# Kernel tuning notes

Measured on AMD Instinct MI355X. Metric: run time of the kernel, lower is better.

The kernel has to match this reference:

```python
import jax, jax.numpy as jnp
import numpy as np

HIDDEN = 2560
N_HEADS = 8
N_KV = 4
HEAD_DIM = 256
SLIDING_WINDOW = 512
SOFTCAP = 50.0
EPS = 1e-6
ROPE_BASE = 10000.0


def setup_inputs() -> dict:
    key = jax.random.key(0)
    ks = jax.random.split(key, 6)
    B, L = 2, 2048
    x = jax.random.normal(ks[0], (B, L, HIDDEN), dtype=jnp.float32)
    mask = jnp.zeros((1, 1, L, L), dtype=jnp.float32)  # additive attention mask
    s = 0.02
    q_w = jax.random.normal(ks[1], (N_HEADS * HEAD_DIM, HIDDEN), dtype=jnp.float32) * s
    k_w = jax.random.normal(ks[2], (N_KV * HEAD_DIM, HIDDEN), dtype=jnp.float32) * s
    v_w = jax.random.normal(ks[3], (N_KV * HEAD_DIM, HIDDEN), dtype=jnp.float32) * s
    o_w = jax.random.normal(ks[4], (HIDDEN, N_HEADS * HEAD_DIM), dtype=jnp.float32) * s
    # Gemma RMSNorm scale initialized to zero (acts as (1 + w))
    q_norm_w = jnp.zeros((HEAD_DIM,), dtype=jnp.float32)
    k_norm_w = jnp.zeros((HEAD_DIM,), dtype=jnp.float32)
    return {"x": x, "mask": mask, "q_w": q_w, "k_w": k_w, "v_w": v_w,
            "o_w": o_w, "q_norm_w": q_norm_w, "k_norm_w": k_norm_w}


def rms_norm(x, w):
    x32 = x.astype(jnp.float32)
    normed = x32 * jax.lax.rsqrt(jnp.mean(x32 * x32, axis=-1, keepdims=True) + EPS)
    return (normed * (1.0 + w)).astype(x.dtype)


def rope_cos_sin(L):
    inv_freq = 1.0 / (ROPE_BASE ** (np.arange(0, HEAD_DIM, 2, dtype=np.float32) / HEAD_DIM))
    t = np.arange(L, dtype=np.float32)
    freqs = np.outer(t, inv_freq)                      # (L, D/2)
    emb = np.concatenate([freqs, freqs], axis=-1)      # (L, D)
    return jnp.asarray(np.cos(emb)), jnp.asarray(np.sin(emb))


def apply_rope(x, cos, sin):
    # x: (B, H, L, D); cos/sin: (L, D)
    half = x.shape[-1] // 2
    rot = jnp.concatenate([-x[..., half:], x[..., :half]], axis=-1)
    return x * cos[None, None] + rot * sin[None, None]


def reference(x, mask, q_w, k_w, v_w, o_w, q_norm_w, k_norm_w):
    B, L, _ = x.shape
    q = (x @ q_w.T).reshape(B, L, N_HEADS, HEAD_DIM).transpose(0, 2, 1, 3)   # (B,Hq,L,D)
    k = (x @ k_w.T).reshape(B, L, N_KV, HEAD_DIM).transpose(0, 2, 1, 3)      # (B,Hkv,L,D)
    v = (x @ v_w.T).reshape(B, L, N_KV, HEAD_DIM).transpose(0, 2, 1, 3)
    q = rms_norm(q, q_norm_w)
    k = rms_norm(k, k_norm_w)
    cos, sin = rope_cos_sin(L)
    q = apply_rope(q, cos, sin)
    k = apply_rope(k, cos, sin)
    groups = N_HEADS // N_KV
    if groups > 1:  # GQA repeat_interleave on head dim
        k = jnp.repeat(k, groups, axis=1)
        v = jnp.repeat(v, groups, axis=1)
    scale = HEAD_DIM ** (-0.5)
    attn_w = jnp.einsum('bhqd,bhkd->bhqk', q, k) * scale
    attn_w = SOFTCAP * jnp.tanh(attn_w / SOFTCAP)
    attn_w = attn_w + mask
    kv_len = attn_w.shape[-1]
    if kv_len > SLIDING_WINDOW:
        # module keeps only the LAST sliding_window key columns for all rows
        col_ok = jnp.arange(kv_len) >= (kv_len - SLIDING_WINDOW)
        attn_w = jnp.where(col_ok[None, None, None, :], attn_w, -jnp.inf)
    attn_w = jax.nn.softmax(attn_w.astype(jnp.float32), axis=-1).astype(q.dtype)
    out = jnp.einsum('bhqk,bhkd->bhqd', attn_w, v)
    out = out.transpose(0, 2, 1, 3).reshape(B, L, N_HEADS * HEAD_DIM)
    return out @ o_w.T
```

## Files before the change

kernel.cpp:

```cpp
#include <hip/hip_runtime.h>
#include <hip/hip_bf16.h>
#include <cstdint>
#include <cmath>


using bf16 = __hip_bfloat16;
typedef __attribute__((ext_vector_type(8))) short short8;
typedef __attribute__((ext_vector_type(4))) float f32x4;

__device__ inline void gl_lds16(const void* g, void* l) {
  __builtin_amdgcn_global_load_lds(
      (const __attribute__((address_space(1))) unsigned int*)g,
      (__attribute__((address_space(3))) unsigned int*)l, 16, 0, 0);
}

__global__ __launch_bounds__(256)
void cvt_qkvx(const float4* __restrict__ x, const float4* __restrict__ qw,
              const float4* __restrict__ kw, const float4* __restrict__ vw,
              __hip_bfloat162* __restrict__ xb, __hip_bfloat162* __restrict__ qkvwb) {
  const int blk = blockIdx.x;
  const float4* src;
  __hip_bfloat162* dstb;
  int i;
  if (blk < 10240) {
    src = x;    dstb = xb;             i = blk * 256 + threadIdx.x;
  } else if (blk < 15360) {
    src = qw;   dstb = qkvwb;          i = (blk - 10240) * 256 + threadIdx.x;
  } else if (blk < 17920) {
    src = kw;   dstb = qkvwb + 2621440; i = (blk - 15360) * 256 + threadIdx.x;
  } else {
    src = vw;   dstb = qkvwb + 3932160; i = (blk - 17920) * 256 + threadIdx.x;
  }
  const float4 v = src[i];
  __hip_bfloat162 lo, hi;
  lo.x = __float2bfloat16(v.x); lo.y = __float2bfloat16(v.y);
  hi.x = __float2bfloat16(v.z); hi.y = __float2bfloat16(v.w);
  dstb[2 * i] = lo;
  dstb[2 * i + 1] = hi;
}

__global__ __launch_bounds__(256)
void cvt_bf16(const float4* __restrict__ in, __hip_bfloat162* __restrict__ out,
              int n4) {
  const int i = blockIdx.x * 256 + threadIdx.x;
  if (i < n4) {
    const float4 v = in[i];
    __hip_bfloat162 lo, hi;
    lo.x = __float2bfloat16(v.x); lo.y = __float2bfloat16(v.y);
    hi.x = __float2bfloat16(v.z); hi.y = __float2bfloat16(v.w);
    out[2 * i] = lo;
    out[2 * i + 1] = hi;
  }
}

template <int EPI>
__global__ __launch_bounds__(512, 2)
void gemm256(const bf16* __restrict__ A, const bf16* __restrict__ B,
             void* __restrict__ C0, void* __restrict__ C1,
             void* __restrict__ C2, int K, int lda, int ldb, int ldc) {
  extern __shared__ short lds[];
  short* As = lds;
  short* Bs = lds + 32768;
  const int t = threadIdx.x;
  const int lane = t & 63;
  const int wid = t >> 6, wm = wid >> 2, wn = wid & 3;
  const int m16 = lane & 15, quad = lane >> 4;
  const int brow = blockIdx.y * 256, bcol = blockIdx.x * 256;

  const int srow = t >> 2;
  const int scol = ((t & 3) ^ ((srow >> 1) & 3)) * 8;
  const bf16* gA0 = A + (size_t)(brow + srow) * lda + scol;
  const bf16* gA1 = A + (size_t)(brow + 128 + srow) * lda + scol;
  const bf16* gB0 = B + (size_t)(bcol + srow) * ldb + scol;
  const bf16* gB1 = B + (size_t)(bcol + 128 + srow) * ldb + scol;
  const int dst = t * 8;

  const int rbA = (wm * 128 + m16) * 32;
  const int rbB = (wn * 64 + m16) * 32;
  const int sw = (quad ^ ((m16 >> 1) & 3)) * 8;

  f32x4 acc[8][4] = {};
  short8 aA[8], aB[8];

  const int nkt = K >> 5;
#pragma unroll
  for (int p = 0; p < 3; ++p) {
    const int o = p * 32;
    short* sa = As + p * 8192;
    short* sb = Bs + p * 8192;
    gl_lds16(gA0 + o, sa + dst);
    gl_lds16(gA1 + o, sa + 4096 + dst);
    gl_lds16(gB0 + o, sb + dst);
    gl_lds16(gB1 + o, sb + 4096 + dst);
  }
  asm volatile("s_waitcnt vmcnt(4)" ::: "memory");
  asm volatile("s_barrier" ::: "memory");
#pragma unroll
  for (int mi = 0; mi < 8; ++mi)
    aA[mi] = *(const short8*)&As[rbA + mi * 512 + sw];

  auto ITER = [&](int j, short8 (&ac)[8], short8 (&an)[8]) {
    if (j + 3 < nkt) {
      const int po = (j + 3) << 5;
      short* pa = As + ((j + 3) & 3) * 8192;
      short* pb = Bs + ((j + 3) & 3) * 8192;
      gl_lds16(gA0 + po, pa + dst);
      gl_lds16(gA1 + po, pa + 4096 + dst);
      gl_lds16(gB0 + po, pb + dst);
      gl_lds16(gB1 + po, pb + 4096 + dst);
    }
    const short* Bb = Bs + (j & 3) * 8192;
    short8 b[4];
#pragma unroll
    for (int nj = 0; nj < 4; ++nj)
      b[nj] = *(const short8*)&Bb[rbB + nj * 512 + sw];
    if (j + 1 < nkt) {
      const short* An = As + ((j + 1) & 3) * 8192;
#pragma unroll
      for (int mi = 0; mi < 8; ++mi)
        an[mi] = *(const short8*)&An[rbA + mi * 512 + sw];
    }
    __builtin_amdgcn_s_setprio(1);
#pragma unroll
    for (int nj = 0; nj < 4; ++nj)
#pragma unroll
      for (int mi = 0; mi < 8; ++mi)
        acc[mi][nj] = __builtin_amdgcn_mfma_f32_16x16x32_bf16(
            ac[mi], b[nj], acc[mi][nj], 0, 0, 0);
    __builtin_amdgcn_s_setprio(0);
    if (j + 4 <= nkt) {
      asm volatile("s_waitcnt vmcnt(4) lgkmcnt(0)" ::: "memory");
    } else if (j + 3 == nkt) {
      asm volatile("s_waitcnt vmcnt(0) lgkmcnt(0)" ::: "memory");
    } else {
      asm volatile("s_waitcnt lgkmcnt(0)" ::: "memory");
    }
    asm volatile("s_barrier" ::: "memory");
  };

  for (int kt = 0; kt < nkt; kt += 2) {
    ITER(kt, aA, aB);
    ITER(kt + 1, aB, aA);
  }

  const int row0 = brow + wm * 128 + quad * 4;
  const int col0 = bcol + wn * 64 + m16;
#pragma unroll
  for (int mi = 0; mi < 8; ++mi) {
#pragma unroll
    for (int ni = 0; ni < 4; ++ni) {
      const int col = col0 + ni * 16;
#pragma unroll
      for (int r = 0; r < 4; ++r) {
        const int row = row0 + mi * 16 + r;
        const float v = acc[mi][ni][r];
        if constexpr (EPI == 0) {
          if (col < 2048) {
            ((bf16*)C0)[(size_t)row * 2048 + col] = __float2bfloat16(v);
          } else if (col < 3072) {
            ((bf16*)C1)[(size_t)row * 1024 + (col - 2048)] = __float2bfloat16(v);
          } else {
            const int b2 = row >> 11;
            ((bf16*)C2)[((size_t)(b2 * 1024 + (col - 3072))) * 2048 +
                        (row & 2047)] = __float2bfloat16(v);
          }
        } else {
          ((float*)C0)[(size_t)row * ldc + col] = v;
        }
      }
    }
  }
}

template <int EPI>
__global__ __launch_bounds__(256)
void gemm(const bf16* __restrict__ A, const bf16* __restrict__ B,
          void* __restrict__ Cv, int K, int lda, int ldb, int ldc,
          long sAh, long sBh, long sCh, float cscale) {
  __shared__ short As[4096];
  __shared__ short Bs[4096];
  const int t = threadIdx.x, lane = t & 63, w = t >> 6;
  const int zh = blockIdx.z;
  A += (size_t)zh * sAh;
  B += (size_t)(zh >> 1) * sBh;
  const size_t coff = (size_t)zh * sCh;
  const int blockRow = blockIdx.y * 128, blockCol = blockIdx.x * 128;

  const int e = t * 8;
  const int srow = t >> 2, scol = (t & 3) * 8;
  const bf16* gA0 = A + (size_t)(blockRow + srow) * lda + scol;
  const bf16* gA1 = gA0 + (size_t)64 * lda;
  const bf16* gB0 = B + (size_t)(blockCol + srow) * ldb + scol;
  const bf16* gB1 = gB0 + (size_t)64 * ldb;

  const int wm = w >> 1, wn = w & 1;
  const int quad = lane >> 4, m16 = lane & 15;
  f32x4 acc[4][4] = {};

  for (int kt = 0; kt < K; kt += 32) {
    __syncthreads();
    gl_lds16(gA0 + kt, &As[e]);
    gl_lds16(gA1 + kt, &As[e + 2048]);
    gl_lds16(gB0 + kt, &Bs[e]);
    gl_lds16(gB1 + kt, &Bs[e + 2048]);
    __syncthreads();
    short8 af[4], bfr[4];
#pragma unroll
    for (int i = 0; i < 4; ++i)
      af[i] = *(const short8*)&As[(wm * 64 + i * 16 + m16) * 32 + quad * 8];
#pragma unroll
    for (int j = 0; j < 4; ++j)
      bfr[j] = *(const short8*)&Bs[(wn * 64 + j * 16 + m16) * 32 + quad * 8];
#pragma unroll
    for (int i = 0; i < 4; ++i)
#pragma unroll
      for (int j = 0; j < 4; ++j)
        acc[i][j] = __builtin_amdgcn_mfma_f32_16x16x32_bf16(af[i], bfr[j],
                                                            acc[i][j], 0, 0, 0);
  }

#pragma unroll
  for (int i = 0; i < 4; ++i) {
#pragma unroll
    for (int j = 0; j < 4; ++j) {
      const int gcol = blockCol + wn * 64 + j * 16 + m16;
#pragma unroll
      for (int r = 0; r < 4; ++r) {
        const int grow = blockRow + wm * 64 + i * 16 + quad * 4 + r;
        float v = acc[i][j][r] * cscale;
        if constexpr (EPI == 1) {
          const float y = v * 0.02f;
          const float ee = __expf(-2.0f * fabsf(y));
          v = copysignf(50.0f * (1.0f - ee) / (1.0f + ee), y);
          ((float*)Cv)[coff + (size_t)grow * ldc + gcol] = v;
        } else {
          ((bf16*)Cv)[coff + (size_t)grow * ldc + gcol] = __float2bfloat16(v);
        }
      }
    }
  }
}

__global__ __launch_bounds__(256)
void norm_rope(bf16* __restrict__ qk, const float* __restrict__ nw, int hmod) {
  const int seg = blockIdx.x * 4 + (threadIdx.x >> 6);
  const int lane = threadIdx.x & 63;
  bf16* p = qk + (size_t)seg * 256;
  float x0 = __bfloat162float(p[lane]);
  float x1 = __bfloat162float(p[lane + 64]);
  float x2 = __bfloat162float(p[lane + 128]);
  float x3 = __bfloat162float(p[lane + 192]);
  float ss = x0 * x0 + x1 * x1 + x2 * x2 + x3 * x3;
#pragma unroll
  for (int o = 32; o; o >>= 1) ss += __shfl_xor(ss, o);
  const float r = rsqrtf(ss * (1.0f / 256.0f) + 1e-6f);
  const float n0 = x0 * r * (1.0f + nw[lane]);
  const float n1 = x1 * r * (1.0f + nw[lane + 64]);
  const float n2 = x2 * r * (1.0f + nw[lane + 128]);
  const float n3 = x3 * r * (1.0f + nw[lane + 192]);
  const int l = (seg / hmod) & 2047;
  const float kf = -9.210340371976184f / 128.0f;
  float c0, s0, c1, s1;
  sincosf((float)l * expf(kf * (float)lane), &s0, &c0);
  sincosf((float)l * expf(kf * (float)(lane + 64)), &s1, &c1);
  p[lane]       = __float2bfloat16(n0 * c0 - n2 * s0);
  p[lane + 128] = __float2bfloat16(n2 * c0 + n0 * s0);
  p[lane + 64]  = __float2bfloat16(n1 * c1 - n3 * s1);
  p[lane + 192] = __float2bfloat16(n3 * c1 + n1 * s1);
}

__global__ __launch_bounds__(256)
void softmax_k(float* __restrict__ S) {
  const int row = blockIdx.x * 4 + (threadIdx.x >> 6);
  const int lane = threadIdx.x & 63;
  float* rowp = S + (size_t)row * 512;
  const float4 a = ((const float4*)rowp)[lane];
  const float4 b = ((const float4*)rowp)[lane + 64];
  float mx = fmaxf(fmaxf(fmaxf(a.x, a.y), fmaxf(a.z, a.w)),
                   fmaxf(fmaxf(b.x, b.y), fmaxf(b.z, b.w)));
#pragma unroll
  for (int o = 32; o; o >>= 1) mx = fmaxf(mx, __shfl_xor(mx, o));
  float e0 = expf(a.x - mx), e1 = expf(a.y - mx);
  float e2 = expf(a.z - mx), e3 = expf(a.w - mx);
  float f0 = expf(b.x - mx), f1 = expf(b.y - mx);
  float f2 = expf(b.z - mx), f3 = expf(b.w - mx);
  float sum = e0 + e1 + e2 + e3 + f0 + f1 + f2 + f3;
#pragma unroll
  for (int o = 32; o; o >>= 1) sum += __shfl_xor(sum, o);
  const float inv = 1.0f / sum;
  bf16* p0 = (bf16*)rowp + lane * 4;
  p0[0] = __float2bfloat16(e0 * inv);
  p0[1] = __float2bfloat16(e1 * inv);
  p0[2] = __float2bfloat16(e2 * inv);
  p0[3] = __float2bfloat16(e3 * inv);
  bf16* p1 = p0 + 256;
  p1[0] = __float2bfloat16(f0 * inv);
  p1[1] = __float2bfloat16(f1 * inv);
  p1[2] = __float2bfloat16(f2 * inv);
  p1[3] = __float2bfloat16(f3 * inv);
}

extern "C" void kernel_launch(void* const* d_in, const int* in_sizes, int n_in,
                              void* d_out, int out_size, void* d_ws, size_t ws_size,
                              hipStream_t stream) {
  const float* x    = (const float*)d_in[0];
  const float* q_w  = (const float*)d_in[2];
  const float* k_w  = (const float*)d_in[3];
  const float* v_w  = (const float*)d_in[4];
  const float* o_w  = (const float*)d_in[5];
  const float* q_nw = (const float*)d_in[6];
  const float* k_nw = (const float*)d_in[7];
  float* out = (float*)d_out;

  char* wsb = (char*)d_ws;
  bf16* xb    = (bf16*)(wsb);
  float* sc   = (float*)(wsb);
  bf16* qkvwb = (bf16*)(wsb + 20971520);
  bf16* owb   = qkvwb;
  bf16* q_ws  = (bf16*)(wsb + 41943040);
  bf16* k_ws  = (bf16*)(wsb + 58720256);
  bf16* vT    = (bf16*)(wsb + 67108864);
  bf16* attn  = q_ws;

  static bool attr_set = false;
  if (!attr_set) {
    (void)hipFuncSetAttribute(reinterpret_cast<const void*>(&gemm256<0>),
                              hipFuncAttributeMaxDynamicSharedMemorySize, 131072);
    (void)hipFuncSetAttribute(reinterpret_cast<const void*>(&gemm256<1>),
                              hipFuncAttributeMaxDynamicSharedMemorySize, 131072);
    attr_set = true;
  }

  dim3 blk(256);
  cvt_qkvx<<<dim3(20480), blk, 0, stream>>>(
      (const float4*)x, (const float4*)q_w, (const float4*)k_w,
      (const float4*)v_w, (__hip_bfloat162*)xb, (__hip_bfloat162*)qkvwb);
  gemm256<0><<<dim3(16, 16), dim3(512), 131072, stream>>>(
      xb, qkvwb, (void*)q_ws, (void*)k_ws, (void*)vT, 2560, 2560, 2560, 0);
  cvt_bf16<<<dim3(5120), blk, 0, stream>>>((const float4*)o_w, (__hip_bfloat162*)owb, 1310720);
  norm_rope<<<dim3(8192), blk, 0, stream>>>(q_ws, q_nw, 8);
  norm_rope<<<dim3(4096), blk, 0, stream>>>(k_ws, k_nw, 4);
  for (int b = 0; b < 2; ++b) {
    for (int c = 0; c < 2; ++c) {
      gemm<1><<<dim3(4, 16, 4), blk, 0, stream>>>(
          q_ws + (size_t)b * 4194304 + c * 1024,
          k_ws + (size_t)b * 2097152 + 1572864 + c * 512,
          (void*)sc, 256, 2048, 1024, 512,
          256L, 256L, 1048576L, 1.0f / 16.0f);
      softmax_k<<<dim3(2048), blk, 0, stream>>>(sc);
      gemm<0><<<dim3(2, 16, 4), blk, 0, stream>>>(
          (const bf16*)sc,
          vT + (size_t)b * 2097152 + (size_t)c * 1048576 + 1536,
          (void*)(attn + (size_t)b * 4194304 + c * 1024), 512, 1024, 2048, 2048,
          2097152L, 524288L, 256L, 1.0f);
    }
  }
  gemm256<1><<<dim3(10, 16), dim3(512), 131072, stream>>>(
      attn, owb, (void*)out, nullptr, nullptr, 2048, 2048, 2048, 2560);
}
```

Measured before the change: 477.3 us.

## Restructure 256x256 GEMM mainloop into BK=64 double-buffered quarter-tile ping-pong

Rewrites the gemm256 main loop to use a 64-wide K tile with two LDS buffers. Each K step is split into four MFMA quadrants, with half-tile global-to-LDS loads and LDS fragment reads interleaved between them and separated by sched barriers. Warp ownership of output rows and columns is remapped into split halves, and the LDS swizzle is widened to 8 chunks. The goal is finer overlap of memory traffic with MFMA work and fewer barriers per unit of K, at the cost of a more intricate waitcnt schedule that could be wrong or stall.

```diff
diff --git a/kernel.cpp b/kernel.cpp
--- a/kernel.cpp
+++ b/kernel.cpp
@@ -67,92 +67,136 @@
   const int m16 = lane & 15, quad = lane >> 4;
   const int brow = blockIdx.y * 256, bcol = blockIdx.x * 256;
 
-  const int srow = t >> 2;
-  const int scol = ((t & 3) ^ ((srow >> 1) & 3)) * 8;
-  const bf16* gA0 = A + (size_t)(brow + srow) * lda + scol;
-  const bf16* gA1 = A + (size_t)(brow + 128 + srow) * lda + scol;
-  const bf16* gB0 = B + (size_t)(bcol + srow) * ldb + scol;
-  const bf16* gB1 = B + (size_t)(bcol + 128 + srow) * ldb + scol;
+  const int srow = t >> 3;
+  const int scol = ((t & 7) ^ (srow & 7)) * 8;
+  const bf16* gA[2][2];
+  const bf16* gB[2][2];
+#pragma unroll
+  for (int h = 0; h < 2; ++h)
+#pragma unroll
+    for (int l = 0; l < 2; ++l) {
+      gA[h][l] = A + (size_t)(brow + h * 128 + l * 64 + srow) * lda + scol;
+      gB[h][l] = B + (size_t)(bcol + h * 128 + l * 64 + srow) * ldb + scol;
+    }
   const int dst = t * 8;
 
-  const int rbA = (wm * 128 + m16) * 32;
-  const int rbB = (wn * 64 + m16) * 32;
-  const int sw = (quad ^ ((m16 >> 1) & 3)) * 8;
+  const int rbA = (wm * 64 + m16) * 64;
+  const int rbB = (wn * 32 + m16) * 64;
+  const int sw0 = ((quad) ^ (m16 & 7)) * 8;
+  const int sw1 = ((4 + quad) ^ (m16 & 7)) * 8;
 
   f32x4 acc[8][4] = {};
-  short8 aA[8], aB[8];
-
-  const int nkt = K >> 5;
-#pragma unroll
-  for (int p = 0; p < 3; ++p) {
-    const int o = p * 32;
-    short* sa = As + p * 8192;
-    short* sb = Bs + p * 8192;
-    gl_lds16(gA0 + o, sa + dst);
-    gl_lds16(gA1 + o, sa + 4096 + dst);
-    gl_lds16(gB0 + o, sb + dst);
-    gl_lds16(gB1 + o, sb + 4096 + dst);
-  }
-  asm volatile("s_waitcnt vmcnt(4)" ::: "memory");
-  asm volatile("s_barrier" ::: "memory");
-#pragma unroll
-  for (int mi = 0; mi < 8; ++mi)
-    aA[mi] = *(const short8*)&As[rbA + mi * 512 + sw];
-
-  auto ITER = [&](int j, short8 (&ac)[8], short8 (&an)[8]) {
-    if (j + 3 < nkt) {
-      const int po = (j + 3) << 5;
-      short* pa = As + ((j + 3) & 3) * 8192;
-      short* pb = Bs + ((j + 3) & 3) * 8192;
-      gl_lds16(gA0 + po, pa + dst);
-      gl_lds16(gA1 + po, pa + 4096 + dst);
-      gl_lds16(gB0 + po, pb + dst);
-      gl_lds16(gB1 + po, pb + 4096 + dst);
-    }
-    const short* Bb = Bs + (j & 3) * 8192;
-    short8 b[4];
-#pragma unroll
-    for (int nj = 0; nj < 4; ++nj)
-      b[nj] = *(const short8*)&Bb[rbB + nj * 512 + sw];
-    if (j + 1 < nkt) {
-      const short* An = As + ((j + 1) & 3) * 8192;
-#pragma unroll
-      for (int mi = 0; mi < 8; ++mi)
-        an[mi] = *(const short8*)&An[rbA + mi * 512 + sw];
-    }
-    __builtin_amdgcn_s_setprio(1);
-#pragma unroll
-    for (int nj = 0; nj < 4; ++nj)
-#pragma unroll
-      for (int mi = 0; mi < 8; ++mi)
-        acc[mi][nj] = __builtin_amdgcn_mfma_f32_16x16x32_bf16(
-            ac[mi], b[nj], acc[mi][nj], 0, 0, 0);
-    __builtin_amdgcn_s_setprio(0);
-    if (j + 4 <= nkt) {
-      asm volatile("s_waitcnt vmcnt(4) lgkmcnt(0)" ::: "memory");
-    } else if (j + 3 == nkt) {
-      asm volatile("s_waitcnt vmcnt(0) lgkmcnt(0)" ::: "memory");
+  short8 aA[8], aB[8], bA[4], bB[4];
+
+#define STAGE_A(bufS, ko, h)                                               \
+  do {                                                                     \
+    gl_lds16(gA[h][0] + (ko), &As[(bufS)*16384 + (h)*8192 + dst]);         \
+    gl_lds16(gA[h][1] + (ko), &As[(bufS)*16384 + (h)*8192 + 4096 + dst]);  \
+  } while (0)
+#define STAGE_B(bufS, ko, h)                                               \
+  do {                                                                     \
+    gl_lds16(gB[h][0] + (ko), &Bs[(bufS)*16384 + (h)*8192 + dst]);         \
+    gl_lds16(gB[h][1] + (ko), &Bs[(bufS)*16384 + (h)*8192 + 4096 + dst]);  \
+  } while (0)
+#define READ_A(dest, bufv, mh)                                             \
+  do {                                                                     \
+    _Pragma("unroll") for (int mi = 0; mi < 4; ++mi) {                     \
+      dest[mi * 2 + 0] = *(const short8*)&As[(bufv)*16384 + (mh)*8192 +    \
+                                             rbA + mi * 1024 + sw0];       \
+      dest[mi * 2 + 1] = *(const short8*)&As[(bufv)*16384 + (mh)*8192 +    \
+                                             rbA + mi * 1024 + sw1];       \
+    }                                                                      \
+  } while (0)
+#define READ_B(dest, bufv, nh)                                             \
+  do {                                                                     \
+    _Pragma("unroll") for (int nj = 0; nj < 2; ++nj) {                     \
+      dest[nj * 2 + 0] = *(const short8*)&Bs[(bufv)*16384 + (nh)*8192 +    \
+                                             rbB + nj * 1024 + sw0];       \
+      dest[nj * 2 + 1] = *(const short8*)&Bs[(bufv)*16384 + (nh)*8192 +    \
+                                             rbB + nj * 1024 + sw1];       \
+    }                                                                      \
+  } while (0)
+#define MFMA_Q(mh, nh, aS, bS)                                             \
+  do {                                                                     \
+    __builtin_amdgcn_s_setprio(1);                                         \
+    _Pragma("unroll") for (int mi = 0; mi < 4; ++mi)                       \
+    _Pragma("unroll") for (int nj = 0; nj < 2; ++nj)                       \
+    _Pragma("unroll") for (int kk = 0; kk < 2; ++kk)                       \
+      acc[(mh)*4 + mi][(nh)*2 + nj] = __builtin_amdgcn_mfma_f32_16x16x32_bf16( \
+          aS[mi * 2 + kk], bS[nj * 2 + kk], acc[(mh)*4 + mi][(nh)*2 + nj], \
+          0, 0, 0);                                                        \
+    __builtin_amdgcn_s_setprio(0);                                         \
+  } while (0)
+#define BAR() asm volatile("s_barrier" ::: "memory")
+#define VM_END()                                                           \
+  do {                                                                     \
+    if (T + 2 < nkt) asm volatile("s_waitcnt vmcnt(8)" ::: "memory");      \
+    else             asm volatile("s_waitcnt vmcnt(0)" ::: "memory");      \
+  } while (0)
+#define SB() __builtin_amdgcn_sched_barrier(0)
+
+  const int nkt = K >> 6;
+  STAGE_A(0, 0, 0);
+  STAGE_B(0, 0, 0);
+  STAGE_B(0, 0, 1);
+  STAGE_A(0, 0, 1);
+  STAGE_A(1, 64, 0);
+  STAGE_B(1, 64, 0);
+  STAGE_B(1, 64, 1);
+  asm volatile("s_waitcnt vmcnt(6)" ::: "memory");
+  BAR();
+  READ_A(aA, 0, 0);
+  READ_B(bA, 0, 0);
+
+  for (int T = 0; T < nkt; ++T) {
+    const int buf = T & 1, nb = buf ^ 1;
+    const int ko1 = (T + 1) << 6, ko2 = (T + 2) << 6;
+
+    READ_B(bB, buf, 1);
+    if (T + 1 < nkt) STAGE_A(nb, ko1, 1);
+    asm volatile("s_waitcnt lgkmcnt(4)" ::: "memory");
+    SB();
+    MFMA_Q(0, 0, aA, bA);
+    VM_END();
+    BAR();
+
+    READ_A(aB, buf, 1);
+    if (T + 2 < nkt) STAGE_A(buf, ko2, 0);
+    asm volatile("s_waitcnt lgkmcnt(8)" ::: "memory");
+    SB();
+    MFMA_Q(0, 1, aA, bB);
+    VM_END();
+    BAR();
+
+    if (T + 1 < nkt) READ_A(aA, nb, 0);
+    if (T + 2 < nkt) STAGE_B(buf, ko2, 0);
+    if (T + 1 < nkt) {
+      asm volatile("s_waitcnt lgkmcnt(8)" ::: "memory");
     } else {
       asm volatile("s_waitcnt lgkmcnt(0)" ::: "memory");
     }
-    asm volatile("s_barrier" ::: "memory");
-  };
-
-  for (int kt = 0; kt < nkt; kt += 2) {
-    ITER(kt, aA, aB);
-    ITER(kt + 1, aB, aA);
-  }
-
-  const int row0 = brow + wm * 128 + quad * 4;
-  const int col0 = bcol + wn * 64 + m16;
+    SB();
+    MFMA_Q(1, 1, aB, bB);
+    VM_END();
+    BAR();
+
+    if (T + 2 < nkt) STAGE_B(buf, ko2, 1);
+    SB();
+    MFMA_Q(1, 0, aB, bA);
+    if (T + 1 < nkt) READ_B(bA, nb, 0);
+    VM_END();
+    BAR();
+  }
+
 #pragma unroll
   for (int mi = 0; mi < 8; ++mi) {
 #pragma unroll
     for (int ni = 0; ni < 4; ++ni) {
-      const int col = col0 + ni * 16;
+      const int col = bcol + (ni >> 1) * 128 + wn * 32 + (ni & 1) * 16 + m16;
 #pragma unroll
       for (int r = 0; r < 4; ++r) {
-        const int row = row0 + mi * 16 + r;
+        const int row =
+            brow + (mi >> 2) * 128 + wm * 64 + (mi & 3) * 16 + quad * 4 + r;
         const float v = acc[mi][ni][r];
         if constexpr (EPI == 0) {
           if (col < 2048) {
@@ -170,6 +214,14 @@
       }
     }
   }
+#undef STAGE_A
+#undef STAGE_B
+#undef READ_A
+#undef READ_B
+#undef MFMA_Q
+#undef BAR
+#undef VM_END
+#undef SB
 }
 
 template <int EPI>
```

Measured after the change: 480.6 us. About the same (+0.7%).
